# Performance work log

Hardware: AMD Instinct MI355X
Metric: run time of the kernel (lower is better)

## Reference

```python
import jax, jax.numpy as jnp
import numpy as np

N, T, D_MODEL, H, DK = 4, 4096, 1024, 16, 64


def setup_inputs() -> dict:
    key = jax.random.key(0)
    ks = jax.random.split(key, 16)
    randn = lambda k, sh: jax.random.normal(k, sh, dtype=jnp.float32)
    # linear weights stored (in, out) so y = x @ W + b (math-equivalent to torch Linear)
    scale = 1.0 / np.sqrt(D_MODEL)
    return {
        "x_k": randn(ks[0], (N, T, D_MODEL)),
        "x_v": randn(ks[1], (N, T, D_MODEL)),
        "x_q": randn(ks[2], (N, T, D_MODEL)),
        "mask": jnp.ones((N, T), dtype=jnp.int32),
        "Wk": randn(ks[3], (D_MODEL, H * DK)) * scale,
        "bk": randn(ks[4], (H * DK,)) * 0.02,
        "Wv": randn(ks[5], (D_MODEL, H * DK)) * scale,
        "bv": randn(ks[6], (H * DK,)) * 0.02,
        "Wq": randn(ks[7], (D_MODEL, H * DK)) * scale,
        "bq": randn(ks[8], (H * DK,)) * 0.02,
        "alpha_w": randn(ks[9], (DK,)),
        "beta_w": randn(ks[10], (DK,)),
        "Wr": randn(ks[11], (DK, DK)) * (1.0 / np.sqrt(DK)),
        "br": randn(ks[12], (DK,)) * 0.02,
        "Wfc": randn(ks[13], (H * DK, D_MODEL)) * scale,
        "bfc": randn(ks[14], (D_MODEL,)) * 0.02,
    }


def _split_heads(x):  # (n, t, h*d) -> (n, h, t, d)
    n, t, _ = x.shape
    return x.reshape(n, t, H, DK).transpose(0, 2, 1, 3)


def reference(x_k, x_v, x_q, mask, Wk, bk, Wv, bv, Wq, bq,
              alpha_w, beta_w, Wr, br, Wfc, bfc):
    scale = DK ** (-0.5)
    k = _split_heads(x_k @ Wk + bk)  # (n, h, t, d)
    v = _split_heads(x_v @ Wv + bv)
    q = _split_heads(x_q @ Wq + bq)

    m = (mask == 0)[:, None, :]  # (n, 1, t) True where masked
    neg_inf = jnp.finfo(q.dtype).min

    # alpha pooling over queries -> global query (n, h, d)
    alpha = jnp.einsum('nhtd,d->nht', q, alpha_w) * scale
    alpha = jnp.where(m, neg_inf, alpha)
    alpha = jax.nn.softmax(alpha, axis=-1)
    global_query = jnp.einsum('nht,nhtd->nhd', alpha, q)

    # p = broadcast(global_query) * k, then beta pooling -> global key
    p = global_query[:, :, None, :] * k  # (n, h, t, d)
    beta = jnp.einsum('nhtd,d->nht', p, beta_w) * scale
    beta = jnp.where(m, neg_inf, beta)
    beta = jax.nn.softmax(beta, axis=-1)
    global_key = jnp.einsum('nht,nhtd->nhd', beta, p)

    u = global_key[:, :, None, :] * v  # (n, h, t, d)
    u_r = u @ Wr + br
    A = u_r + q  # (n, h, t, d)
    A = A.transpose(0, 2, 1, 3).reshape(N, T, H * DK)
    return A @ Wfc + bfc
```

## Files before the change

### kernel.cpp

```cpp
#include <hip/hip_runtime.h>

typedef __bf16 bf16x8 __attribute__((ext_vector_type(8)));
typedef float f32x4 __attribute__((ext_vector_type(4)));
typedef unsigned int u32x4 __attribute__((ext_vector_type(4)));
typedef unsigned short u16x4 __attribute__((ext_vector_type(4)));
typedef unsigned short u16x8 __attribute__((ext_vector_type(8)));

#define SEQ_T 4096
#define DMODEL 1024
#define HEADS 16
#define DKH 64
#define MTOK 16384

#define AS1 __attribute__((address_space(1)))
#define AS3 __attribute__((address_space(3)))

__device__ __forceinline__ unsigned short f2bf(float f) {
  unsigned u = __builtin_bit_cast(unsigned int, f);
  u += 0x7FFFu + ((u >> 16) & 1u);
  return (unsigned short)(u >> 16);
}
__device__ __forceinline__ float bf2f(unsigned short h) {
  unsigned u = ((unsigned)h) << 16;
  return __builtin_bit_cast(float, u);
}
__device__ __forceinline__ void gload16(const unsigned short* g, unsigned short* l) {
  __builtin_amdgcn_global_load_lds((const AS1 unsigned int*)(g),
                                   (AS3 unsigned int*)(l), 16, 0, 0);
}

__global__ void __launch_bounds__(256) k_cvt(const float* __restrict__ x,
                                             unsigned short* __restrict__ y,
                                             long long nelem) {
  long long i = ((long long)blockIdx.x * 256 + threadIdx.x) * 8;
  if (i >= nelem) return;
  u16x8 o;
#pragma unroll
  for (int j = 0; j < 8; ++j) o[j] = f2bf(x[i + j]);
  *(u16x8*)(y + i) = o;
}

__global__ void __launch_bounds__(256) k_wtrans(const float* __restrict__ W,
                                                unsigned short* __restrict__ Wt,
                                                int K, int N) {
  __shared__ float tile[32][33];
  int bn = blockIdx.x * 32, bk = blockIdx.y * 32;
  int tx = threadIdx.x, ty = threadIdx.y;
#pragma unroll
  for (int j = 0; j < 32; j += 8)
    tile[ty + j][tx] = W[(size_t)(bk + ty + j) * N + bn + tx];
  __syncthreads();
#pragma unroll
  for (int j = 0; j < 32; j += 8)
    Wt[(size_t)(bn + ty + j) * K + bk + tx] = f2bf(tile[tx][ty + j]);
}

#define BM 128
#define BN 128
#define BK 32

template <int OBF, int SCORE>
__global__ void __launch_bounds__(256, 2)
k_gemm(const unsigned short* __restrict__ A, const unsigned short* __restrict__ Bt,
       const float* __restrict__ bias, void* __restrict__ C,
       const int* __restrict__ mask, const float* __restrict__ swt,
       float* __restrict__ sbuf, int M, int N, int K) {
  __shared__ unsigned short As[BM * BK];
  __shared__ unsigned short Bs[BN * BK];
  const int tid = threadIdx.x;
  const int lane = tid & 63, wid = tid >> 6;
  const int wr = wid >> 1, wc = wid & 1;
  const int bnb = blockIdx.x;
  const int bm = blockIdx.y * BM, bn = bnb * BN;
  const int l15 = lane & 15, l4 = lane >> 4;

  f32x4 acc[4][4];
#pragma unroll
  for (int i = 0; i < 4; ++i)
#pragma unroll
    for (int j = 0; j < 4; ++j)
#pragma unroll
      for (int e = 0; e < 4; ++e) acc[i][j][e] = 0.f;

  const int srow = wid * 32 + (lane >> 2);
  const int scol = (lane & 3) * 8;
  const unsigned short* Ag = A + (size_t)(bm + srow) * K + scol;
  const unsigned short* Bg = Bt + (size_t)(bn + srow) * K + scol;
  unsigned short* Al = As + wid * 32 * BK;
  unsigned short* Bl = Bs + wid * 32 * BK;

  for (int kt = 0; kt < K; kt += BK) {
    __syncthreads();
    gload16(Ag + kt, Al);
    gload16(Ag + kt + 16 * K, Al + 16 * BK);
    gload16(Bg + kt, Bl);
    gload16(Bg + kt + 16 * K, Bl + 16 * BK);
    __syncthreads();
    bf16x8 af[4], bfr[4];
#pragma unroll
    for (int m = 0; m < 4; ++m)
      af[m] = *(const bf16x8*)(As + (wr * 64 + m * 16 + l15) * BK + l4 * 8);
#pragma unroll
    for (int n = 0; n < 4; ++n)
      bfr[n] = *(const bf16x8*)(Bs + (wc * 64 + n * 16 + l15) * BK + l4 * 8);
#pragma unroll
    for (int m = 0; m < 4; ++m)
#pragma unroll
      for (int n = 0; n < 4; ++n)
        acc[m][n] = __builtin_amdgcn_mfma_f32_16x16x32_bf16(af[m], bfr[n],
                                                            acc[m][n], 0, 0, 0);
  }

  const int crow = bm + wr * 64 + l4 * 4;
  const int ccol = bn + wc * 64 + l15;

  float pacc[4][4];
  const float* wrow = nullptr;
  if (SCORE == 1) wrow = swt;
  if (SCORE == 2) wrow = swt + ((size_t)((bm >> 12) * HEADS + bnb * 2 + wc)) * DKH;
  if (SCORE) {
#pragma unroll
    for (int m = 0; m < 4; ++m)
#pragma unroll
      for (int e = 0; e < 4; ++e) pacc[m][e] = 0.f;
  }

#pragma unroll
  for (int m = 0; m < 4; ++m)
#pragma unroll
    for (int n = 0; n < 4; ++n) {
      int c = ccol + n * 16;
      float bj = bias[c];
      float wg = SCORE ? wrow[n * 16 + l15] : 0.f;
#pragma unroll
      for (int e = 0; e < 4; ++e) {
        int r = crow + m * 16 + e;
        float v = acc[m][n][e] + bj;
        if (SCORE) pacc[m][e] += v * wg;
        if (OBF)
          ((unsigned short*)C)[(size_t)r * N + c] = f2bf(v);
        else
          ((float*)C)[(size_t)r * N + c] = v;
      }
    }

  if (SCORE) {
#pragma unroll
    for (int m = 0; m < 4; ++m)
#pragma unroll
      for (int e = 0; e < 4; ++e) {
        float p = pacc[m][e];
        p += __shfl_xor(p, 1);
        p += __shfl_xor(p, 2);
        p += __shfl_xor(p, 4);
        p += __shfl_xor(p, 8);
        if (l15 == 0) {
          int r = crow + m * 16 + e;
          int t = r & (SEQ_T - 1), n = r >> 12;
          float sc = p * 0.125f;
          if (mask[n * SEQ_T + t] == 0) sc = -3.0e38f;
          sbuf[((size_t)n * HEADS + bnb * 2 + wc) * SEQ_T + t] = sc;
        }
      }
  }
}

__global__ void __launch_bounds__(256) k_stat1(const float* __restrict__ s,
                                               float* __restrict__ pmax,
                                               float* __restrict__ psum) {
  __shared__ float red[4];
  const int b = blockIdx.x, tid = threadIdx.x, lane = tid & 63, wid = tid >> 6;
  float v = s[(size_t)b * 256 + tid];
  float m = v;
#pragma unroll
  for (int o = 1; o < 64; o <<= 1) m = fmaxf(m, __shfl_xor(m, o));
  if (lane == 0) red[wid] = m;
  __syncthreads();
  m = fmaxf(fmaxf(red[0], red[1]), fmaxf(red[2], red[3]));
  __syncthreads();
  float e = __expf(v - m);
#pragma unroll
  for (int o = 1; o < 64; o <<= 1) e += __shfl_xor(e, o);
  if (lane == 0) red[wid] = e;
  __syncthreads();
  if (tid == 0) {
    pmax[b] = m;
    psum[b] = red[0] + red[1] + red[2] + red[3];
  }
}

__global__ void __launch_bounds__(64) k_stat2(const float* __restrict__ pmax,
                                              const float* __restrict__ psum,
                                              float* __restrict__ smx,
                                              float* __restrict__ sinv) {
  const int b = blockIdx.x, lane = threadIdx.x;
  float pm = -3.4e38f, ps = 0.f;
  if (lane < 16) {
    pm = pmax[b * 16 + lane];
    ps = psum[b * 16 + lane];
  }
  float gm = pm;
#pragma unroll
  for (int o = 1; o < 16; o <<= 1) gm = fmaxf(gm, __shfl_xor(gm, o));
  float sc = ps * __expf(pm - gm);
#pragma unroll
  for (int o = 1; o < 16; o <<= 1) sc += __shfl_xor(sc, o);
  if (lane == 0) {
    smx[b] = gm;
    sinv[b] = 1.f / sc;
  }
}

__global__ void __launch_bounds__(256) k_wsum(const unsigned short* __restrict__ X,
                                              const float* __restrict__ s,
                                              const float* __restrict__ mxv,
                                              const float* __restrict__ invv,
                                              float* __restrict__ pbuf) {
  __shared__ float part[16][64];
  const int nh = blockIdx.x >> 4, chunk = blockIdx.x & 15;
  const int n = nh >> 4, h = nh & 15;
  const int tid = threadIdx.x, lane = tid & 63, wid = tid >> 6;
  const int tsub = lane >> 4, dl = lane & 15;
  const float mx = mxv[nh], inv = invv[nh];
  const float* sb = s + (size_t)nh * SEQ_T + chunk * 256;
  const size_t base = ((size_t)n * SEQ_T + chunk * 256) * DMODEL + h * DKH + dl * 4;
  f32x4 acc = {0.f, 0.f, 0.f, 0.f};
  for (int t = wid * 4 + tsub; t < 256; t += 16) {
    float w = __expf(sb[t] - mx) * inv;
    u16x4 xv = *(const u16x4*)(X + base + (size_t)t * DMODEL);
    acc[0] += w * bf2f(xv[0]);
    acc[1] += w * bf2f(xv[1]);
    acc[2] += w * bf2f(xv[2]);
    acc[3] += w * bf2f(xv[3]);
  }
  int g = wid * 4 + tsub;
#pragma unroll
  for (int e = 0; e < 4; ++e) part[g][dl * 4 + e] = acc[e];
  __syncthreads();
  if (tid < 64) {
    float v = 0.f;
#pragma unroll
    for (int gg = 0; gg < 16; ++gg) v += part[gg][tid];
    pbuf[(size_t)blockIdx.x * 64 + tid] = v;
  }
}

template <int MODE>
__global__ void __launch_bounds__(64) k_fin(const float* __restrict__ pbuf,
                                            const float* __restrict__ gq,
                                            const float* __restrict__ bw,
                                            float* __restrict__ out,
                                            float* __restrict__ wv) {
  const int nh = blockIdx.x, d = threadIdx.x;
  float v = 0.f;
#pragma unroll
  for (int c = 0; c < 16; ++c) v += pbuf[((size_t)nh * 16 + c) * 64 + d];
  if (MODE == 1) v *= gq[(size_t)nh * 64 + d];
  out[(size_t)nh * 64 + d] = v;
  if (MODE == 0) wv[(size_t)nh * 64 + d] = v * bw[d];
}

__global__ void __launch_bounds__(256) k_wrg(const float* __restrict__ gk,
                                             const float* __restrict__ Wr,
                                             unsigned short* __restrict__ WrgT) {
  const int nh = blockIdx.x, tid = threadIdx.x;
#pragma unroll
  for (int i = 0; i < 16; ++i) {
    int idx = i * 256 + tid;
    int d = idx >> 6, dd = idx & 63;
    WrgT[(size_t)nh * 4096 + idx] = f2bf(gk[nh * 64 + dd] * Wr[dd * 64 + d]);
  }
}

#define ABM 128
#define VLD 72
__global__ void __launch_bounds__(256) k_abuild2(const unsigned short* __restrict__ v,
                                                 const unsigned short* __restrict__ qbf,
                                                 const unsigned short* __restrict__ WrgT,
                                                 const float* __restrict__ br,
                                                 unsigned short* __restrict__ A) {
  __shared__ unsigned short Vs[ABM * VLD];
  __shared__ unsigned short Ws[DKH * VLD];
  const int tid = threadIdx.x, lane = tid & 63, wid = tid >> 6;
  const int nh = blockIdx.y;
  const int n = nh >> 4, h = nh & 15;
  const size_t nt0 = (size_t)n * SEQ_T + (size_t)blockIdx.x * ABM;
  const size_t vbase = nt0 * DMODEL + (size_t)h * DKH;
#pragma unroll
  for (int p = 0; p < 4; ++p) {
    int idx = p * 256 + tid;
    int row = idx >> 3, c = idx & 7;
    *(u32x4*)(Vs + row * VLD + c * 8) =
        *(const u32x4*)(v + vbase + (size_t)row * DMODEL + c * 8);
  }
#pragma unroll
  for (int p = 0; p < 2; ++p) {
    int idx = p * 256 + tid;
    int row = idx >> 3, c = idx & 7;
    *(u32x4*)(Ws + row * VLD + c * 8) =
        *(const u32x4*)(WrgT + (size_t)nh * 4096 + row * 64 + c * 8);
  }
  __syncthreads();
  const int l15 = lane & 15, l4 = lane >> 4;
  f32x4 acc[2][4];
#pragma unroll
  for (int m = 0; m < 2; ++m)
#pragma unroll
    for (int nf = 0; nf < 4; ++nf)
#pragma unroll
      for (int e = 0; e < 4; ++e) acc[m][nf][e] = 0.f;
#pragma unroll
  for (int ks = 0; ks < 2; ++ks) {
    bf16x8 af[2], bfr[4];
#pragma unroll
    for (int m = 0; m < 2; ++m)
      af[m] = *(const bf16x8*)(Vs + (wid * 32 + m * 16 + l15) * VLD + l4 * 8 + ks * 32);
#pragma unroll
    for (int nf = 0; nf < 4; ++nf)
      bfr[nf] = *(const bf16x8*)(Ws + (nf * 16 + l15) * VLD + l4 * 8 + ks * 32);
#pragma unroll
    for (int m = 0; m < 2; ++m)
#pragma unroll
      for (int nf = 0; nf < 4; ++nf)
        acc[m][nf] = __builtin_amdgcn_mfma_f32_16x16x32_bf16(af[m], bfr[nf],
                                                             acc[m][nf], 0, 0, 0);
  }
#pragma unroll
  for (int m = 0; m < 2; ++m)
#pragma unroll
    for (int nf = 0; nf < 4; ++nf) {
      int d = nf * 16 + l15;
      float bj = br[d];
#pragma unroll
      for (int e = 0; e < 4; ++e) {
        int r = wid * 32 + m * 16 + l4 * 4 + e;
        size_t off = vbase + (size_t)r * DMODEL + d;
        float val = acc[m][nf][e] + bj + bf2f(qbf[off]);
        A[off] = f2bf(val);
      }
    }
}

extern "C" void kernel_launch(void* const* d_in, const int* in_sizes, int n_in,
                              void* d_out, int out_size, void* d_ws, size_t ws_size,
                              hipStream_t stream) {
  const float* x_k = (const float*)d_in[0];
  const float* x_v = (const float*)d_in[1];
  const float* x_q = (const float*)d_in[2];
  const int* mask = (const int*)d_in[3];
  const float* Wk = (const float*)d_in[4];
  const float* bk = (const float*)d_in[5];
  const float* Wv = (const float*)d_in[6];
  const float* bv = (const float*)d_in[7];
  const float* Wq = (const float*)d_in[8];
  const float* bq = (const float*)d_in[9];
  const float* alpha_w = (const float*)d_in[10];
  const float* beta_w = (const float*)d_in[11];
  const float* Wr = (const float*)d_in[12];
  const float* br = (const float*)d_in[13];
  const float* Wfc = (const float*)d_in[14];
  const float* bfc = (const float*)d_in[15];

  unsigned short* qbf = (unsigned short*)d_out;

  char* ws = (char*)d_ws;
  const size_t SZ_XBF = (size_t)MTOK * DMODEL * 2;
  unsigned short* kbf = (unsigned short*)(ws);
  unsigned short* vbf = (unsigned short*)(ws + SZ_XBF);
  unsigned short* xst = (unsigned short*)(ws + 2 * SZ_XBF);
  unsigned short* WkT = (unsigned short*)(ws + 3 * SZ_XBF);
  unsigned short* WvT = WkT + (size_t)DMODEL * DMODEL;
  unsigned short* WqT = WvT + (size_t)DMODEL * DMODEL;
  unsigned short* WfT = WqT + (size_t)DMODEL * DMODEL;
  unsigned short* WrgT = WfT + (size_t)DMODEL * DMODEL;
  float* gq = (float*)(WrgT + (size_t)64 * 4096);
  float* gk = gq + 4096;
  float* wvb = gk + 4096;
  float* sbuf = wvb + 4096;
  float* pbuf = sbuf + (size_t)64 * SEQ_T;
  float* pmax = pbuf + 1024 * 64;
  float* psum = pmax + 1024;
  float* smx = psum + 1024;
  float* sinv = smx + 64;

  dim3 tb(32, 8);
  dim3 tg(DMODEL / 32, DMODEL / 32);
  k_wtrans<<<tg, tb, 0, stream>>>(Wq, WqT, DMODEL, DMODEL);
  k_wtrans<<<tg, tb, 0, stream>>>(Wk, WkT, DMODEL, DMODEL);
  k_wtrans<<<tg, tb, 0, stream>>>(Wv, WvT, DMODEL, DMODEL);
  k_wtrans<<<tg, tb, 0, stream>>>(Wfc, WfT, DMODEL, DMODEL);

  long long nx = (long long)MTOK * DMODEL;
  int cvtg = (int)(nx / 8 / 256);
  dim3 ggrid(DMODEL / BN, MTOK / BM);

  k_cvt<<<cvtg, 256, 0, stream>>>(x_q, xst, nx);
  k_gemm<1, 1><<<ggrid, 256, 0, stream>>>(xst, WqT, bq, (void*)qbf, mask, alpha_w,
                                          sbuf, MTOK, DMODEL, DMODEL);
  k_stat1<<<1024, 256, 0, stream>>>(sbuf, pmax, psum);
  k_stat2<<<64, 64, 0, stream>>>(pmax, psum, smx, sinv);
  k_wsum<<<1024, 256, 0, stream>>>(qbf, sbuf, smx, sinv, pbuf);
  k_fin<0><<<64, 64, 0, stream>>>(pbuf, nullptr, beta_w, gq, wvb);

  k_cvt<<<cvtg, 256, 0, stream>>>(x_k, xst, nx);
  k_gemm<1, 2><<<ggrid, 256, 0, stream>>>(xst, WkT, bk, (void*)kbf, mask, wvb,
                                          sbuf, MTOK, DMODEL, DMODEL);
  k_stat1<<<1024, 256, 0, stream>>>(sbuf, pmax, psum);
  k_stat2<<<64, 64, 0, stream>>>(pmax, psum, smx, sinv);
  k_wsum<<<1024, 256, 0, stream>>>(kbf, sbuf, smx, sinv, pbuf);
  k_fin<1><<<64, 64, 0, stream>>>(pbuf, gq, nullptr, gk, nullptr);

  k_cvt<<<cvtg, 256, 0, stream>>>(x_v, xst, nx);
  k_gemm<1, 0><<<ggrid, 256, 0, stream>>>(xst, WvT, bv, (void*)vbf, nullptr, nullptr,
                                          nullptr, MTOK, DMODEL, DMODEL);

  k_wrg<<<64, 256, 0, stream>>>(gk, Wr, WrgT);
  dim3 agrid(SEQ_T / ABM, 64);
  k_abuild2<<<agrid, 256, 0, stream>>>(vbf, qbf, WrgT, br, xst);

  k_gemm<0, 0><<<ggrid, 256, 0, stream>>>(xst, WfT, bfc, d_out, nullptr, nullptr,
                                          nullptr, MTOK, DMODEL, DMODEL);
}
```

Measured before the change: 328.4 us.

## Fuse fp32-to-bf16 conversion into larger double-buffered swizzled GEMM

Removes the separate fp32-to-bf16 conversion kernels and has the GEMM load fp32 activations directly, converting them in registers before writing to LDS. The GEMM moves to 256x256x64 tiles with 512 threads, double-buffered LDS with an XOR-swizzled layout, prefetch of the next K tile during MFMA, and a remapped workgroup order. It targets the extra memory round trip of the conversion passes and low per-block data reuse. In exchange it uses more registers and LDS per block, leaves fewer blocks in the grid (256), and the fp32 loads sit in registers across the compute phase.

```diff
diff --git a/kernel.cpp b/kernel.cpp
--- a/kernel.cpp
+++ b/kernel.cpp
@@ -27,17 +27,6 @@
 __device__ __forceinline__ void gload16(const unsigned short* g, unsigned short* l) {
   __builtin_amdgcn_global_load_lds((const AS1 unsigned int*)(g),
                                    (AS3 unsigned int*)(l), 16, 0, 0);
-}
-
-__global__ void __launch_bounds__(256) k_cvt(const float* __restrict__ x,
-                                             unsigned short* __restrict__ y,
-                                             long long nelem) {
-  long long i = ((long long)blockIdx.x * 256 + threadIdx.x) * 8;
-  if (i >= nelem) return;
-  u16x8 o;
-#pragma unroll
-  for (int j = 0; j < 8; ++j) o[j] = f2bf(x[i + j]);
-  *(u16x8*)(y + i) = o;
 }
 
 __global__ void __launch_bounds__(256) k_wtrans(const float* __restrict__ W,
@@ -55,87 +44,165 @@
     Wt[(size_t)(bn + ty + j) * K + bk + tx] = f2bf(tile[tx][ty + j]);
 }
 
-#define BM 128
-#define BN 128
-#define BK 32
-
-template <int OBF, int SCORE>
-__global__ void __launch_bounds__(256, 2)
-k_gemm(const unsigned short* __restrict__ A, const unsigned short* __restrict__ Bt,
+#define BM 256
+#define BN 256
+#define BK 64
+
+template <int OBF, int SCORE, int AF32>
+__global__ void __launch_bounds__(512, 2)
+k_gemm(const void* __restrict__ Ain, const unsigned short* __restrict__ Bt,
        const float* __restrict__ bias, void* __restrict__ C,
        const int* __restrict__ mask, const float* __restrict__ swt,
        float* __restrict__ sbuf, int M, int N, int K) {
-  __shared__ unsigned short As[BM * BK];
-  __shared__ unsigned short Bs[BN * BK];
+  __shared__ unsigned short Asb[2][BM * BK];
+  __shared__ unsigned short Bsb[2][BN * BK];
   const int tid = threadIdx.x;
   const int lane = tid & 63, wid = tid >> 6;
-  const int wr = wid >> 1, wc = wid & 1;
-  const int bnb = blockIdx.x;
-  const int bm = blockIdx.y * BM, bn = bnb * BN;
+  const int wr = wid >> 2, wc = wid & 3;
   const int l15 = lane & 15, l4 = lane >> 4;
 
-  f32x4 acc[4][4];
-#pragma unroll
-  for (int i = 0; i < 4; ++i)
+  const int nwg = gridDim.x * gridDim.y;
+  const int flat = blockIdx.x + blockIdx.y * gridDim.x;
+  const int rm = (flat & 7) * (nwg >> 3) + (flat >> 3);
+  const int bx = rm % gridDim.x, by = rm / gridDim.x;
+  const int bm = by * BM, bn = bx * BN;
+
+  const float* Af = (const float*)Ain;
+  const unsigned short* Abf = (const unsigned short*)Ain;
+
+  f32x4 acc[8][4];
+#pragma unroll
+  for (int i = 0; i < 8; ++i)
 #pragma unroll
     for (int j = 0; j < 4; ++j)
 #pragma unroll
       for (int e = 0; e < 4; ++e) acc[i][j][e] = 0.f;
 
-  const int srow = wid * 32 + (lane >> 2);
-  const int scol = (lane & 3) * 8;
-  const unsigned short* Ag = A + (size_t)(bm + srow) * K + scol;
-  const unsigned short* Bg = Bt + (size_t)(bn + srow) * K + scol;
-  unsigned short* Al = As + wid * 32 * BK;
-  unsigned short* Bl = Bs + wid * 32 * BK;
-
-  for (int kt = 0; kt < K; kt += BK) {
-    __syncthreads();
-    gload16(Ag + kt, Al);
-    gload16(Ag + kt + 16 * K, Al + 16 * BK);
-    gload16(Bg + kt, Bl);
-    gload16(Bg + kt + 16 * K, Bl + 16 * BK);
-    __syncthreads();
-    bf16x8 af[4], bfr[4];
-#pragma unroll
-    for (int m = 0; m < 4; ++m)
-      af[m] = *(const bf16x8*)(As + (wr * 64 + m * 16 + l15) * BK + l4 * 8);
-#pragma unroll
-    for (int n = 0; n < 4; ++n)
-      bfr[n] = *(const bf16x8*)(Bs + (wc * 64 + n * 16 + l15) * BK + l4 * 8);
-#pragma unroll
-    for (int m = 0; m < 4; ++m)
-#pragma unroll
-      for (int n = 0; n < 4; ++n)
-        acc[m][n] = __builtin_amdgcn_mfma_f32_16x16x32_bf16(af[m], bfr[n],
-                                                            acc[m][n], 0, 0, 0);
-  }
-
-  const int crow = bm + wr * 64 + l4 * 4;
+  const int sgr = lane >> 3;
+  const int sgc = (lane & 7) ^ sgr;
+  const int r0 = tid >> 3;
+  const int c7l = tid & 7;
+  const int c7s = c7l ^ (r0 & 7);
+
+  f32x4 alo[4], ahi[4];
+  auto loadA32 = [&](int t) {
+#pragma unroll
+    for (int s = 0; s < 4; ++s) {
+      const float* src = Af + (size_t)(bm + r0 + s * 64) * K + t * BK + c7s * 8;
+      alo[s] = *(const f32x4*)src;
+      ahi[s] = *(const f32x4*)(src + 4);
+    }
+  };
+  auto writeA32 = [&](int t) {
+    unsigned short* dst = &Asb[t & 1][0];
+#pragma unroll
+    for (int s = 0; s < 4; ++s) {
+      u16x8 o;
+#pragma unroll
+      for (int j = 0; j < 4; ++j) {
+        o[j] = f2bf(alo[s][j]);
+        o[4 + j] = f2bf(ahi[s][j]);
+      }
+      *(u16x8*)(dst + (r0 + s * 64) * BK + c7l * 8) = o;
+    }
+  };
+  auto stageAbf = [&](int t) {
+    unsigned short* dst = &Asb[t & 1][0];
+#pragma unroll
+    for (int j = 0; j < 4; ++j) {
+      int g = wid * 4 + j;
+      gload16(Abf + (size_t)(bm + g * 8 + sgr) * K + t * BK + sgc * 8,
+              dst + g * 512);
+    }
+  };
+  auto stageB = [&](int t) {
+    unsigned short* dst = &Bsb[t & 1][0];
+#pragma unroll
+    for (int j = 0; j < 4; ++j) {
+      int g = wid * 4 + j;
+      gload16(Bt + (size_t)(bn + g * 8 + sgr) * K + t * BK + sgc * 8,
+              dst + g * 512);
+    }
+  };
+
+  const int nt = K / BK;
+  if (AF32) {
+    loadA32(0);
+    writeA32(0);
+  } else {
+    stageAbf(0);
+  }
+  stageB(0);
+
+  for (int t = 0; t < nt; ++t) {
+    asm volatile("s_waitcnt vmcnt(0)" ::: "memory");
+    asm volatile("s_waitcnt lgkmcnt(0)" ::: "memory");
+    __builtin_amdgcn_s_barrier();
+    const bool pf = (t + 1 < nt);
+    if (pf) {
+      if (AF32) loadA32(t + 1); else stageAbf(t + 1);
+      stageB(t + 1);
+    }
+    const unsigned short* Ab = &Asb[t & 1][0];
+    const unsigned short* Bb = &Bsb[t & 1][0];
+#pragma unroll
+    for (int ks = 0; ks < 2; ++ks) {
+      bf16x8 bfr[4];
+#pragma unroll
+      for (int nf = 0; nf < 4; ++nf) {
+        int rowb = wc * 64 + nf * 16 + l15;
+        int c7 = (ks * 4 + l4) ^ (rowb & 7);
+        bfr[nf] = *(const bf16x8*)(Bb + rowb * BK + c7 * 8);
+      }
+#pragma unroll
+      for (int mh = 0; mh < 2; ++mh) {
+        bf16x8 af[4];
+#pragma unroll
+        for (int i = 0; i < 4; ++i) {
+          int rowa = wr * 128 + (mh * 4 + i) * 16 + l15;
+          int c7 = (ks * 4 + l4) ^ (rowa & 7);
+          af[i] = *(const bf16x8*)(Ab + rowa * BK + c7 * 8);
+        }
+        __builtin_amdgcn_s_setprio(1);
+#pragma unroll
+        for (int i = 0; i < 4; ++i)
+#pragma unroll
+          for (int nf = 0; nf < 4; ++nf)
+            acc[mh * 4 + i][nf] = __builtin_amdgcn_mfma_f32_16x16x32_bf16(
+                af[i], bfr[nf], acc[mh * 4 + i][nf], 0, 0, 0);
+        __builtin_amdgcn_s_setprio(0);
+      }
+    }
+    if (pf && AF32) writeA32(t + 1);
+    asm volatile("s_waitcnt lgkmcnt(0)" ::: "memory");
+    __builtin_amdgcn_s_barrier();
+  }
+
+  const int crow = bm + wr * 128 + l4 * 4;
   const int ccol = bn + wc * 64 + l15;
-
-  float pacc[4][4];
+  float pacc[8][4];
   const float* wrow = nullptr;
   if (SCORE == 1) wrow = swt;
-  if (SCORE == 2) wrow = swt + ((size_t)((bm >> 12) * HEADS + bnb * 2 + wc)) * DKH;
+  if (SCORE == 2)
+    wrow = swt + ((size_t)((bm >> 12) * HEADS + bx * 4 + wc)) * DKH;
   if (SCORE) {
 #pragma unroll
-    for (int m = 0; m < 4; ++m)
+    for (int m = 0; m < 8; ++m)
 #pragma unroll
       for (int e = 0; e < 4; ++e) pacc[m][e] = 0.f;
   }
 
 #pragma unroll
-  for (int m = 0; m < 4; ++m)
-#pragma unroll
-    for (int n = 0; n < 4; ++n) {
-      int c = ccol + n * 16;
+  for (int m = 0; m < 8; ++m)
+#pragma unroll
+    for (int nf = 0; nf < 4; ++nf) {
+      int c = ccol + nf * 16;
       float bj = bias[c];
-      float wg = SCORE ? wrow[n * 16 + l15] : 0.f;
+      float wg = SCORE ? wrow[nf * 16 + l15] : 0.f;
 #pragma unroll
       for (int e = 0; e < 4; ++e) {
         int r = crow + m * 16 + e;
-        float v = acc[m][n][e] + bj;
+        float v = acc[m][nf][e] + bj;
         if (SCORE) pacc[m][e] += v * wg;
         if (OBF)
           ((unsigned short*)C)[(size_t)r * N + c] = f2bf(v);
@@ -146,7 +213,7 @@
 
   if (SCORE) {
 #pragma unroll
-    for (int m = 0; m < 4; ++m)
+    for (int m = 0; m < 8; ++m)
 #pragma unroll
       for (int e = 0; e < 4; ++e) {
         float p = pacc[m][e];
@@ -159,7 +226,7 @@
           int t = r & (SEQ_T - 1), n = r >> 12;
           float sc = p * 0.125f;
           if (mask[n * SEQ_T + t] == 0) sc = -3.0e38f;
-          sbuf[((size_t)n * HEADS + bnb * 2 + wc) * SEQ_T + t] = sc;
+          sbuf[((size_t)n * HEADS + bx * 4 + wc) * SEQ_T + t] = sc;
         }
       }
   }
@@ -390,34 +457,29 @@
   k_wtrans<<<tg, tb, 0, stream>>>(Wv, WvT, DMODEL, DMODEL);
   k_wtrans<<<tg, tb, 0, stream>>>(Wfc, WfT, DMODEL, DMODEL);
 
-  long long nx = (long long)MTOK * DMODEL;
-  int cvtg = (int)(nx / 8 / 256);
   dim3 ggrid(DMODEL / BN, MTOK / BM);
 
-  k_cvt<<<cvtg, 256, 0, stream>>>(x_q, xst, nx);
-  k_gemm<1, 1><<<ggrid, 256, 0, stream>>>(xst, WqT, bq, (void*)qbf, mask, alpha_w,
-                                          sbuf, MTOK, DMODEL, DMODEL);
+  k_gemm<1, 1, 1><<<ggrid, 512, 0, stream>>>(x_q, WqT, bq, (void*)qbf, mask,
+                                             alpha_w, sbuf, MTOK, DMODEL, DMODEL);
   k_stat1<<<1024, 256, 0, stream>>>(sbuf, pmax, psum);
   k_stat2<<<64, 64, 0, stream>>>(pmax, psum, smx, sinv);
   k_wsum<<<1024, 256, 0, stream>>>(qbf, sbuf, smx, sinv, pbuf);
   k_fin<0><<<64, 64, 0, stream>>>(pbuf, nullptr, beta_w, gq, wvb);
 
-  k_cvt<<<cvtg, 256, 0, stream>>>(x_k, xst, nx);
-  k_gemm<1, 2><<<ggrid, 256, 0, stream>>>(xst, WkT, bk, (void*)kbf, mask, wvb,
-                                          sbuf, MTOK, DMODEL, DMODEL);
+  k_gemm<1, 2, 1><<<ggrid, 512, 0, stream>>>(x_k, WkT, bk, (void*)kbf, mask,
+                                             wvb, sbuf, MTOK, DMODEL, DMODEL);
   k_stat1<<<1024, 256, 0, stream>>>(sbuf, pmax, psum);
   k_stat2<<<64, 64, 0, stream>>>(pmax, psum, smx, sinv);
   k_wsum<<<1024, 256, 0, stream>>>(kbf, sbuf, smx, sinv, pbuf);
   k_fin<1><<<64, 64, 0, stream>>>(pbuf, gq, nullptr, gk, nullptr);
 
-  k_cvt<<<cvtg, 256, 0, stream>>>(x_v, xst, nx);
-  k_gemm<1, 0><<<ggrid, 256, 0, stream>>>(xst, WvT, bv, (void*)vbf, nullptr, nullptr,
-                                          nullptr, MTOK, DMODEL, DMODEL);
+  k_gemm<1, 0, 1><<<ggrid, 512, 0, stream>>>(x_v, WvT, bv, (void*)vbf, nullptr,
+                                             nullptr, nullptr, MTOK, DMODEL, DMODEL);
 
   k_wrg<<<64, 256, 0, stream>>>(gk, Wr, WrgT);
   dim3 agrid(SEQ_T / ABM, 64);
   k_abuild2<<<agrid, 256, 0, stream>>>(vbf, qbf, WrgT, br, xst);
 
-  k_gemm<0, 0><<<ggrid, 256, 0, stream>>>(xst, WfT, bfc, d_out, nullptr, nullptr,
-                                          nullptr, MTOK, DMODEL, DMODEL);
-}
+  k_gemm<0, 0, 0><<<ggrid, 512, 0, stream>>>(xst, WfT, bfc, d_out, nullptr,
+                                             nullptr, nullptr, MTOK, DMODEL, DMODEL);
+}
```

Measured after the change: 297.6 us. -9.4%, faster.

## Fuse fp32-to-bf16 input conversion into GEMM A-loading with swizzled BK=64 tiles

Applied to the files above, without the earlier changes.

Removes the three separate conversion kernels. The GEMM now loads fp32 activations directly, prefetching the next tile into registers and converting to bf16 while writing LDS. It also doubles BK to 64, XOR-swizzles the LDS layout to avoid bank conflicts, and remaps workgroup ids to spread tiles across XCDs. This trades an extra read/write pass over the activations for higher register pressure and fp32 global reads inside the GEMM.

```diff
diff --git a/kernel.cpp b/kernel.cpp
--- a/kernel.cpp
+++ b/kernel.cpp
@@ -14,6 +14,7 @@
 
 #define AS1 __attribute__((address_space(1)))
 #define AS3 __attribute__((address_space(3)))
+#define MEMFENCE asm volatile("" ::: "memory")
 
 __device__ __forceinline__ unsigned short f2bf(float f) {
   unsigned u = __builtin_bit_cast(unsigned int, f);
@@ -27,17 +28,6 @@
 __device__ __forceinline__ void gload16(const unsigned short* g, unsigned short* l) {
   __builtin_amdgcn_global_load_lds((const AS1 unsigned int*)(g),
                                    (AS3 unsigned int*)(l), 16, 0, 0);
-}
-
-__global__ void __launch_bounds__(256) k_cvt(const float* __restrict__ x,
-                                             unsigned short* __restrict__ y,
-                                             long long nelem) {
-  long long i = ((long long)blockIdx.x * 256 + threadIdx.x) * 8;
-  if (i >= nelem) return;
-  u16x8 o;
-#pragma unroll
-  for (int j = 0; j < 8; ++j) o[j] = f2bf(x[i + j]);
-  *(u16x8*)(y + i) = o;
 }
 
 __global__ void __launch_bounds__(256) k_wtrans(const float* __restrict__ W,
@@ -57,11 +47,11 @@
 
 #define BM 128
 #define BN 128
-#define BK 32
-
-template <int OBF, int SCORE>
+#define BK 64
+
+template <int OBF, int SCORE, int AF32>
 __global__ void __launch_bounds__(256, 2)
-k_gemm(const unsigned short* __restrict__ A, const unsigned short* __restrict__ Bt,
+k_gemm(const void* __restrict__ Ain, const unsigned short* __restrict__ Bt,
        const float* __restrict__ bias, void* __restrict__ C,
        const int* __restrict__ mask, const float* __restrict__ swt,
        float* __restrict__ sbuf, int M, int N, int K) {
@@ -70,10 +60,18 @@
   const int tid = threadIdx.x;
   const int lane = tid & 63, wid = tid >> 6;
   const int wr = wid >> 1, wc = wid & 1;
-  const int bnb = blockIdx.x;
-  const int bm = blockIdx.y * BM, bn = bnb * BN;
   const int l15 = lane & 15, l4 = lane >> 4;
 
+  const int nwg = gridDim.x * gridDim.y;
+  const int flat = blockIdx.x + blockIdx.y * gridDim.x;
+  const int rm = (flat & 7) * (nwg >> 3) + (flat >> 3);
+  const int bx = rm % gridDim.x, by = rm / gridDim.x;
+  const int bm = by * BM, bn = bx * BN;
+
+  const float* Af = (const float*)Ain;
+  const unsigned short* Abf = (const unsigned short*)Ain;
+  const int nt = K / BK;
+
   f32x4 acc[4][4];
 #pragma unroll
   for (int i = 0; i < 4; ++i)
@@ -82,42 +80,90 @@
 #pragma unroll
       for (int e = 0; e < 4; ++e) acc[i][j][e] = 0.f;
 
-  const int srow = wid * 32 + (lane >> 2);
-  const int scol = (lane & 3) * 8;
-  const unsigned short* Ag = A + (size_t)(bm + srow) * K + scol;
-  const unsigned short* Bg = Bt + (size_t)(bn + srow) * K + scol;
-  unsigned short* Al = As + wid * 32 * BK;
-  unsigned short* Bl = Bs + wid * 32 * BK;
-
-  for (int kt = 0; kt < K; kt += BK) {
+  const int sgr = lane >> 3;
+  const int sgc = (lane & 7) ^ sgr;
+  const int r0 = tid >> 2;
+  const int c4 = tid & 3;
+  f32x4 alv[2][4];
+
+  auto stageB = [&](int t) {
+#pragma unroll
+    for (int j = 0; j < 4; ++j) {
+      int g = wid * 4 + j;
+      gload16(Bt + (size_t)(bn + g * 8 + sgr) * K + t * BK + sgc * 8,
+              Bs + g * 512);
+    }
+  };
+  auto stageAbf = [&](int t) {
+#pragma unroll
+    for (int j = 0; j < 4; ++j) {
+      int g = wid * 4 + j;
+      gload16(Abf + (size_t)(bm + g * 8 + sgr) * K + t * BK + sgc * 8,
+              As + g * 512);
+    }
+  };
+  auto aload = [&](int t) {
+#pragma unroll
+    for (int s = 0; s < 2; ++s) {
+      const float* src = Af + (size_t)(bm + r0 + s * 64) * K + t * BK + c4 * 16;
+#pragma unroll
+      for (int j = 0; j < 4; ++j) alv[s][j] = *(const f32x4*)(src + j * 4);
+    }
+  };
+  auto awrite = [&]() {
+#pragma unroll
+    for (int s = 0; s < 2; ++s) {
+      int row = r0 + s * 64;
+#pragma unroll
+      for (int half = 0; half < 2; ++half) {
+        u16x8 o;
+#pragma unroll
+        for (int j = 0; j < 8; ++j) o[j] = f2bf(alv[s][half * 2 + (j >> 2)][j & 3]);
+        int ch = (c4 * 2 + half) ^ (row & 7);
+        *(u16x8*)(As + row * BK + ch * 8) = o;
+      }
+    }
+  };
+
+  if (AF32) aload(0);
+
+  for (int t = 0; t < nt; ++t) {
     __syncthreads();
-    gload16(Ag + kt, Al);
-    gload16(Ag + kt + 16 * K, Al + 16 * BK);
-    gload16(Bg + kt, Bl);
-    gload16(Bg + kt + 16 * K, Bl + 16 * BK);
+    if (AF32) awrite();
+    else stageAbf(t);
+    stageB(t);
     __syncthreads();
-    bf16x8 af[4], bfr[4];
-#pragma unroll
-    for (int m = 0; m < 4; ++m)
-      af[m] = *(const bf16x8*)(As + (wr * 64 + m * 16 + l15) * BK + l4 * 8);
-#pragma unroll
-    for (int n = 0; n < 4; ++n)
-      bfr[n] = *(const bf16x8*)(Bs + (wc * 64 + n * 16 + l15) * BK + l4 * 8);
-#pragma unroll
-    for (int m = 0; m < 4; ++m)
-#pragma unroll
-      for (int n = 0; n < 4; ++n)
-        acc[m][n] = __builtin_amdgcn_mfma_f32_16x16x32_bf16(af[m], bfr[n],
-                                                            acc[m][n], 0, 0, 0);
+#pragma unroll
+    for (int kh = 0; kh < 2; ++kh) {
+      bf16x8 af[4], bfr[4];
+#pragma unroll
+      for (int m = 0; m < 4; ++m) {
+        int ra = wr * 64 + m * 16 + l15;
+        int c7 = (kh * 4 + l4) ^ (ra & 7);
+        af[m] = *(const bf16x8*)(As + ra * BK + c7 * 8);
+      }
+#pragma unroll
+      for (int n = 0; n < 4; ++n) {
+        int rb = wc * 64 + n * 16 + l15;
+        int c7 = (kh * 4 + l4) ^ (rb & 7);
+        bfr[n] = *(const bf16x8*)(Bs + rb * BK + c7 * 8);
+      }
+      if (AF32 && kh == 0 && t + 1 < nt) aload(t + 1);
+#pragma unroll
+      for (int m = 0; m < 4; ++m)
+#pragma unroll
+        for (int n = 0; n < 4; ++n)
+          acc[m][n] = __builtin_amdgcn_mfma_f32_16x16x32_bf16(af[m], bfr[n],
+                                                              acc[m][n], 0, 0, 0);
+    }
   }
 
   const int crow = bm + wr * 64 + l4 * 4;
   const int ccol = bn + wc * 64 + l15;
-
   float pacc[4][4];
   const float* wrow = nullptr;
   if (SCORE == 1) wrow = swt;
-  if (SCORE == 2) wrow = swt + ((size_t)((bm >> 12) * HEADS + bnb * 2 + wc)) * DKH;
+  if (SCORE == 2) wrow = swt + ((size_t)((bm >> 12) * HEADS + bx * 2 + wc)) * DKH;
   if (SCORE) {
 #pragma unroll
     for (int m = 0; m < 4; ++m)
@@ -156,10 +202,10 @@
         p += __shfl_xor(p, 8);
         if (l15 == 0) {
           int r = crow + m * 16 + e;
-          int t = r & (SEQ_T - 1), n = r >> 12;
+          int tt = r & (SEQ_T - 1), n = r >> 12;
           float sc = p * 0.125f;
-          if (mask[n * SEQ_T + t] == 0) sc = -3.0e38f;
-          sbuf[((size_t)n * HEADS + bnb * 2 + wc) * SEQ_T + t] = sc;
+          if (mask[n * SEQ_T + tt] == 0) sc = -3.0e38f;
+          sbuf[((size_t)n * HEADS + bx * 2 + wc) * SEQ_T + tt] = sc;
         }
       }
   }
@@ -390,34 +436,29 @@
   k_wtrans<<<tg, tb, 0, stream>>>(Wv, WvT, DMODEL, DMODEL);
   k_wtrans<<<tg, tb, 0, stream>>>(Wfc, WfT, DMODEL, DMODEL);
 
-  long long nx = (long long)MTOK * DMODEL;
-  int cvtg = (int)(nx / 8 / 256);
   dim3 ggrid(DMODEL / BN, MTOK / BM);
 
-  k_cvt<<<cvtg, 256, 0, stream>>>(x_q, xst, nx);
-  k_gemm<1, 1><<<ggrid, 256, 0, stream>>>(xst, WqT, bq, (void*)qbf, mask, alpha_w,
-                                          sbuf, MTOK, DMODEL, DMODEL);
+  k_gemm<1, 1, 1><<<ggrid, 256, 0, stream>>>(x_q, WqT, bq, (void*)qbf, mask,
+                                             alpha_w, sbuf, MTOK, DMODEL, DMODEL);
   k_stat1<<<1024, 256, 0, stream>>>(sbuf, pmax, psum);
   k_stat2<<<64, 64, 0, stream>>>(pmax, psum, smx, sinv);
   k_wsum<<<1024, 256, 0, stream>>>(qbf, sbuf, smx, sinv, pbuf);
   k_fin<0><<<64, 64, 0, stream>>>(pbuf, nullptr, beta_w, gq, wvb);
 
-  k_cvt<<<cvtg, 256, 0, stream>>>(x_k, xst, nx);
-  k_gemm<1, 2><<<ggrid, 256, 0, stream>>>(xst, WkT, bk, (void*)kbf, mask, wvb,
-                                          sbuf, MTOK, DMODEL, DMODEL);
+  k_gemm<1, 2, 1><<<ggrid, 256, 0, stream>>>(x_k, WkT, bk, (void*)kbf, mask,
+                                             wvb, sbuf, MTOK, DMODEL, DMODEL);
   k_stat1<<<1024, 256, 0, stream>>>(sbuf, pmax, psum);
   k_stat2<<<64, 64, 0, stream>>>(pmax, psum, smx, sinv);
   k_wsum<<<1024, 256, 0, stream>>>(kbf, sbuf, smx, sinv, pbuf);
   k_fin<1><<<64, 64, 0, stream>>>(pbuf, gq, nullptr, gk, nullptr);
 
-  k_cvt<<<cvtg, 256, 0, stream>>>(x_v, xst, nx);
-  k_gemm<1, 0><<<ggrid, 256, 0, stream>>>(xst, WvT, bv, (void*)vbf, nullptr, nullptr,
-                                          nullptr, MTOK, DMODEL, DMODEL);
+  k_gemm<1, 0, 1><<<ggrid, 256, 0, stream>>>(x_v, WvT, bv, (void*)vbf, nullptr,
+                                             nullptr, nullptr, MTOK, DMODEL, DMODEL);
 
   k_wrg<<<64, 256, 0, stream>>>(gk, Wr, WrgT);
   dim3 agrid(SEQ_T / ABM, 64);
   k_abuild2<<<agrid, 256, 0, stream>>>(vbf, qbf, WrgT, br, xst);
 
-  k_gemm<0, 0><<<ggrid, 256, 0, stream>>>(xst, WfT, bfc, d_out, nullptr, nullptr,
-                                          nullptr, MTOK, DMODEL, DMODEL);
-}
+  k_gemm<0, 0, 0><<<ggrid, 256, 0, stream>>>(xst, WfT, bfc, d_out, nullptr,
+                                             nullptr, nullptr, MTOK, DMODEL, DMODEL);
+}
```

After: 331.3 us. No clear change (+0.9%).
